# Kernel optimization log

Hardware: AMD Instinct MI355X
Metric: run time of the kernel (lower is better)

## Reference

```python
import jax, jax.numpy as jnp
import numpy as np

N_FILTERS = 1024
KH, KW = 5, 5
LOC = 3                      # locality (pad + maxpool kernel/stride)
B, H, W = 1024, 64, 64
WIN = KH + 2 * LOC           # 11: sliced window side after padding


def setup_inputs() -> dict:
    key = jax.random.key(0)
    k1, k2, k3, k4 = jax.random.split(key, 4)
    X = jax.random.normal(k1, (B, 1, H, W), dtype=jnp.float32)
    weight = jax.random.normal(k2, (N_FILTERS, 1, KH, KW), dtype=jnp.float32)
    bias = jax.random.normal(k3, (N_FILTERS,), dtype=jnp.float32)
    # top-left corner (i, j) of each filter's window in the padded image;
    # must satisfy i + KH + 2*LOC <= H + 2*LOC  =>  i in [0, H-KH]
    positions = jax.random.randint(k4, (N_FILTERS, 2), 0, H - KH + 1, dtype=jnp.int32)
    return {"X": X, "weight": weight, "bias": bias, "positions": positions}


def reference(X, weight, bias, positions):
    # ZeroPad2d(locality)
    Xp = jnp.pad(X, ((0, 0), (0, 0), (LOC, LOC), (LOC, LOC)))

    def slice_one(pos):
        return jax.lax.dynamic_slice(Xp, (0, 0, pos[0], pos[1]), (B, 1, WIN, WIN))

    windows = jax.vmap(slice_one)(positions)
    lhs = jnp.transpose(windows[:, :, 0], (1, 0, 2, 3))

    # All n_filters tiny single-channel convs as ONE grouped conv.
    conv = jax.lax.conv_general_dilated(
        lhs, weight, window_strides=(1, 1), padding='VALID',
        dimension_numbers=('NCHW', 'OIHW', 'NCHW'),
        feature_group_count=N_FILTERS)                # [B,F,2L+1,2L+1] = [B,F,7,7]
    conv = conv + bias[None, :, None, None]

    # MaxPool2d((LOC,LOC)) with default stride=LOC, floor mode -> 2x2.
    pooled = jax.lax.reduce_window(
        conv, -jnp.inf, jax.lax.max,
        window_dimensions=(1, 1, LOC, LOC),
        window_strides=(1, 1, LOC, LOC),
        padding='VALID')                              # [B,F,2,2]

    # torch.cat(dim=1) over per-filter [B,1,2,2] tensors + reshape(B,-1)
    return pooled.reshape(B, -1)                      # [B, F*4]
```

## Files before the change

kernel.cpp:

```cpp
#include <hip/hip_runtime.h>

#define N_FILTERS 1024
#define B_TOTAL   1024
#define IMG       64
#define PAD_DIM   70

typedef _Float16 half2_t __attribute__((ext_vector_type(2)));
typedef float    fvec2   __attribute__((ext_vector_type(2)));

__global__ __launch_bounds__(256) void prep_kernel(
    const float* __restrict__ X, _Float16* __restrict__ Xt)
{
    if (blockIdx.x < 512) {
        __shared__ float T[128 * 65];
        const int pt = blockIdx.x & 63;
        const int bt = blockIdx.x >> 6;
        const int tx = threadIdx.x & 63, ty = threadIdx.x >> 6;

        #pragma unroll
        for (int pass = 0; pass < 32; ++pass) {
            int bl = pass * 4 + ty;
            T[bl * 65 + tx] = X[(size_t)(bt * 128 + bl) * 4096 + pt * 64 + tx];
        }
        __syncthreads();
        #pragma unroll
        for (int pass = 0; pass < 16; ++pass) {
            int pl = pass * 4 + ty;
            int p  = pt * 64 + pl;
            int r  = p >> 6, c = p & 63;
            half2_t h;
            h.x = (_Float16)T[(2 * tx) * 65 + pl];
            h.y = (_Float16)T[(2 * tx + 1) * 65 + pl];
            *(half2_t*)&Xt[(size_t)((r + 3) * PAD_DIM + (c + 3)) * 1024 + bt * 128 + 2 * tx] = h;
        }
    } else {
        const int bp = blockIdx.x - 512;
        for (int pp = bp; pp < PAD_DIM * PAD_DIM; pp += 64) {
            int r = pp / PAD_DIM, c = pp - r * PAD_DIM;
            if (r >= 3 && r < 67 && c >= 3 && c < 67) continue;
            unsigned int* q = (unsigned int*)Xt + (size_t)pp * 512;
            q[threadIdx.x] = 0u;
            q[threadIdx.x + 256] = 0u;
        }
    }
}

__global__ __launch_bounds__(256, 2) void filters_main(
    const _Float16* __restrict__ Xt,
    const float*    __restrict__ W,
    const float*    __restrict__ bias,
    const int*      __restrict__ pos,
    float4*         __restrict__ out4)
{
    const int t    = threadIdx.x;
    const int lane = t & 63;
    const int w    = t >> 6;
    const int bg   = blockIdx.x & 3;
    const int fg   = blockIdx.x >> 2;

    const int f  = fg * 4 + w;
    const int sf = __builtin_amdgcn_readfirstlane(f);
    const int si = __builtin_amdgcn_readfirstlane(pos[2 * sf]);
    const int sj = __builtin_amdgcn_readfirstlane(pos[2 * sf + 1]);

    float wk[25];
    const float* wp = W + sf * 25;
    #pragma unroll
    for (int k = 0; k < 25; ++k) wk[k] = wp[k];

    const int laneByte = bg * 512 + lane * 8;

    fvec2 a0[36], a1[36];
    #pragma unroll
    for (int k = 0; k < 36; ++k) { a0[k] = (fvec2)0.0f; a1[k] = (fvec2)0.0f; }

    #pragma unroll
    for (int wr = 0; wr < 10; ++wr) {
        const char* rowp = (const char*)Xt
                         + (size_t)((si + wr) * PAD_DIM + sj) * 2048 + laneByte;
        fvec2 inA[10], inB[10];
        #pragma unroll
        for (int wc = 0; wc < 10; ++wc) {
            half2_t lo, hi;
            uint2 d = *(const uint2*)(rowp + (size_t)wc * 2048);
            lo = __builtin_bit_cast(half2_t, d.x);
            hi = __builtin_bit_cast(half2_t, d.y);
            inA[wc].x = (float)lo.x; inA[wc].y = (float)lo.y;
            inB[wc].x = (float)hi.x; inB[wc].y = (float)hi.y;
        }
        #pragma unroll
        for (int y = 0; y < 6; ++y) {
            if (y >= ((wr > 4) ? (wr - 4) : 0) && y <= ((wr < 5) ? wr : 5)) {
                const int r = wr - y;
                #pragma unroll
                for (int x = 0; x < 6; ++x) {
                    #pragma unroll
                    for (int c = 0; c < 5; ++c) {
                        a0[y * 6 + x] = wk[r * 5 + c] * inA[x + c] + a0[y * 6 + x];
                        a1[y * 6 + x] = wk[r * 5 + c] * inB[x + c] + a1[y * 6 + x];
                    }
                }
            }
        }
    }

    const float bv = bias[sf];
    float4 o0, o1;
    {
        fvec2 m0[4], m1[4];
        #pragma unroll
        for (int py = 0; py < 2; ++py) {
            #pragma unroll
            for (int px = 0; px < 2; ++px) {
                fvec2 u = a0[(3 * py) * 6 + 3 * px];
                fvec2 v = a1[(3 * py) * 6 + 3 * px];
                #pragma unroll
                for (int dy = 0; dy < 3; ++dy)
                    #pragma unroll
                    for (int dx = 0; dx < 3; ++dx) {
                        fvec2 e0 = a0[(3 * py + dy) * 6 + (3 * px + dx)];
                        fvec2 e1 = a1[(3 * py + dy) * 6 + (3 * px + dx)];
                        u.x = fmaxf(u.x, e0.x); u.y = fmaxf(u.y, e0.y);
                        v.x = fmaxf(v.x, e1.x); v.y = fmaxf(v.y, e1.y);
                    }
                m0[py * 2 + px].x = u.x + bv; m0[py * 2 + px].y = u.y + bv;
                m1[py * 2 + px].x = v.x + bv; m1[py * 2 + px].y = v.y + bv;
            }
        }
        const int b0 = bg * 256 + lane * 4;
        float4 o;
        o.x = m0[0].x; o.y = m0[1].x; o.z = m0[2].x; o.w = m0[3].x;
        out4[(size_t)b0 * 1024 + f] = o;
        o.x = m0[0].y; o.y = m0[1].y; o.z = m0[2].y; o.w = m0[3].y;
        out4[(size_t)(b0 + 1) * 1024 + f] = o;
        o.x = m1[0].x; o.y = m1[1].x; o.z = m1[2].x; o.w = m1[3].x;
        out4[(size_t)(b0 + 2) * 1024 + f] = o;
        o.x = m1[0].y; o.y = m1[1].y; o.z = m1[2].y; o.w = m1[3].y;
        out4[(size_t)(b0 + 3) * 1024 + f] = o;
        (void)o0; (void)o1;
    }
}

extern "C" void kernel_launch(void* const* d_in, const int* in_sizes, int n_in,
                              void* d_out, int out_size, void* d_ws, size_t ws_size,
                              hipStream_t stream) {
    const float* X    = (const float*)d_in[0];
    const float* W    = (const float*)d_in[1];
    const float* bias = (const float*)d_in[2];
    const int*   pos  = (const int*)d_in[3];
    float4* out4 = (float4*)d_out;
    _Float16* Xt = (_Float16*)d_ws;

    prep_kernel<<<576, 256, 0, stream>>>(X, Xt);
    filters_main<<<1024, 256, 0, stream>>>(Xt, W, bias, pos, out4);
}
```

Before: 104.1 us.

## Split pooled output rows across waves and halve batch per lane to cut registers

Each wave now computes a single pooled row (py) for one filter and 2 batch items per lane, where before it computed both pooled rows for 4 batch items. This cuts the accumulators from 72 float2 to 18 and allows 4 blocks per CU instead of 2, with the grid growing to 4096 blocks. The cost is redundant work: the convolution row ranges overlap (7 input rows per wave instead of 10 shared across both pooled rows), each batch-row load is smaller (4 bytes per lane), and the output stores become 8-byte writes.

```diff
diff --git a/kernel.cpp b/kernel.cpp
--- a/kernel.cpp
+++ b/kernel.cpp
@@ -45,100 +45,86 @@
     }
 }
 
-__global__ __launch_bounds__(256, 2) void filters_main(
+__global__ __launch_bounds__(256, 4) void filters_main(
     const _Float16* __restrict__ Xt,
     const float*    __restrict__ W,
     const float*    __restrict__ bias,
     const int*      __restrict__ pos,
-    float4*         __restrict__ out4)
+    float*          __restrict__ out)
 {
     const int t    = threadIdx.x;
     const int lane = t & 63;
-    const int w    = t >> 6;
-    const int bg   = blockIdx.x & 3;
-    const int fg   = blockIdx.x >> 2;
+    const int py   = (t >> 6) & 1;
+    const int fl   = t >> 7;
+    const int bg   = blockIdx.x & 7;
+    const int fg   = blockIdx.x >> 3;
 
-    const int f  = fg * 4 + w;
+    const int f  = fg * 2 + fl;
     const int sf = __builtin_amdgcn_readfirstlane(f);
     const int si = __builtin_amdgcn_readfirstlane(pos[2 * sf]);
     const int sj = __builtin_amdgcn_readfirstlane(pos[2 * sf + 1]);
+    const int r0 = si + 3 * py;
 
     float wk[25];
     const float* wp = W + sf * 25;
     #pragma unroll
     for (int k = 0; k < 25; ++k) wk[k] = wp[k];
 
-    const int laneByte = bg * 512 + lane * 8;
+    const int laneByte = bg * 256 + lane * 4;
 
-    fvec2 a0[36], a1[36];
+    fvec2 acc[18];
     #pragma unroll
-    for (int k = 0; k < 36; ++k) { a0[k] = (fvec2)0.0f; a1[k] = (fvec2)0.0f; }
+    for (int k = 0; k < 18; ++k) acc[k] = (fvec2)0.0f;
 
     #pragma unroll
-    for (int wr = 0; wr < 10; ++wr) {
+    for (int wrl = 0; wrl < 7; ++wrl) {
         const char* rowp = (const char*)Xt
-                         + (size_t)((si + wr) * PAD_DIM + sj) * 2048 + laneByte;
-        fvec2 inA[10], inB[10];
+                         + (size_t)((r0 + wrl) * PAD_DIM + sj) * 2048 + laneByte;
+        fvec2 in2[10];
         #pragma unroll
         for (int wc = 0; wc < 10; ++wc) {
-            half2_t lo, hi;
-            uint2 d = *(const uint2*)(rowp + (size_t)wc * 2048);
-            lo = __builtin_bit_cast(half2_t, d.x);
-            hi = __builtin_bit_cast(half2_t, d.y);
-            inA[wc].x = (float)lo.x; inA[wc].y = (float)lo.y;
-            inB[wc].x = (float)hi.x; inB[wc].y = (float)hi.y;
+            half2_t h = __builtin_bit_cast(half2_t,
+                          *(const unsigned int*)(rowp + (size_t)wc * 2048));
+            in2[wc].x = (float)h.x;
+            in2[wc].y = (float)h.y;
         }
         #pragma unroll
-        for (int y = 0; y < 6; ++y) {
-            if (y >= ((wr > 4) ? (wr - 4) : 0) && y <= ((wr < 5) ? wr : 5)) {
-                const int r = wr - y;
+        for (int y = 0; y < 3; ++y) {
+            if (y >= ((wrl > 4) ? (wrl - 4) : 0) && y <= ((wrl < 2) ? wrl : 2)) {
+                const int r = wrl - y;
                 #pragma unroll
                 for (int x = 0; x < 6; ++x) {
                     #pragma unroll
-                    for (int c = 0; c < 5; ++c) {
-                        a0[y * 6 + x] = wk[r * 5 + c] * inA[x + c] + a0[y * 6 + x];
-                        a1[y * 6 + x] = wk[r * 5 + c] * inB[x + c] + a1[y * 6 + x];
-                    }
+                    for (int c = 0; c < 5; ++c)
+                        acc[y * 6 + x] = wk[r * 5 + c] * in2[x + c] + acc[y * 6 + x];
                 }
             }
         }
     }
 
     const float bv = bias[sf];
-    float4 o0, o1;
-    {
-        fvec2 m0[4], m1[4];
+    fvec2 m[2];
+    #pragma unroll
+    for (int px = 0; px < 2; ++px) {
+        fvec2 u = acc[3 * px];
         #pragma unroll
-        for (int py = 0; py < 2; ++py) {
+        for (int y = 0; y < 3; ++y)
             #pragma unroll
-            for (int px = 0; px < 2; ++px) {
-                fvec2 u = a0[(3 * py) * 6 + 3 * px];
-                fvec2 v = a1[(3 * py) * 6 + 3 * px];
-                #pragma unroll
-                for (int dy = 0; dy < 3; ++dy)
-                    #pragma unroll
-                    for (int dx = 0; dx < 3; ++dx) {
-                        fvec2 e0 = a0[(3 * py + dy) * 6 + (3 * px + dx)];
-                        fvec2 e1 = a1[(3 * py + dy) * 6 + (3 * px + dx)];
-                        u.x = fmaxf(u.x, e0.x); u.y = fmaxf(u.y, e0.y);
-                        v.x = fmaxf(v.x, e1.x); v.y = fmaxf(v.y, e1.y);
-                    }
-                m0[py * 2 + px].x = u.x + bv; m0[py * 2 + px].y = u.y + bv;
-                m1[py * 2 + px].x = v.x + bv; m1[py * 2 + px].y = v.y + bv;
+            for (int dx = 0; dx < 3; ++dx) {
+                fvec2 e = acc[y * 6 + 3 * px + dx];
+                u.x = fmaxf(u.x, e.x);
+                u.y = fmaxf(u.y, e.y);
             }
-        }
-        const int b0 = bg * 256 + lane * 4;
-        float4 o;
-        o.x = m0[0].x; o.y = m0[1].x; o.z = m0[2].x; o.w = m0[3].x;
-        out4[(size_t)b0 * 1024 + f] = o;
-        o.x = m0[0].y; o.y = m0[1].y; o.z = m0[2].y; o.w = m0[3].y;
-        out4[(size_t)(b0 + 1) * 1024 + f] = o;
-        o.x = m1[0].x; o.y = m1[1].x; o.z = m1[2].x; o.w = m1[3].x;
-        out4[(size_t)(b0 + 2) * 1024 + f] = o;
-        o.x = m1[0].y; o.y = m1[1].y; o.z = m1[2].y; o.w = m1[3].y;
-        out4[(size_t)(b0 + 3) * 1024 + f] = o;
-        (void)o0; (void)o1;
+        m[px].x = u.x + bv;
+        m[px].y = u.y + bv;
     }
+
+    const int b0 = bg * 128 + lane * 2;
+    const size_t o0 = (size_t)b0 * 4096 + sf * 4 + py * 2;
+    fvec2 s0; s0.x = m[0].x; s0.y = m[1].x;
+    fvec2 s1; s1.x = m[0].y; s1.y = m[1].y;
+    *(fvec2*)&out[o0]        = s0;
+    *(fvec2*)&out[o0 + 4096] = s1;
 }
 
 extern "C" void kernel_launch(void* const* d_in, const int* in_sizes, int n_in,
@@ -148,9 +134,9 @@
     const float* W    = (const float*)d_in[1];
     const float* bias = (const float*)d_in[2];
     const int*   pos  = (const int*)d_in[3];
-    float4* out4 = (float4*)d_out;
+    float* out = (float*)d_out;
     _Float16* Xt = (_Float16*)d_ws;
 
     prep_kernel<<<576, 256, 0, stream>>>(X, Xt);
-    filters_main<<<1024, 256, 0, stream>>>(Xt, W, bias, pos, out4);
+    filters_main<<<4096, 256, 0, stream>>>(Xt, W, bias, pos, out);
 }
```

Result: no change. 104.5 us (+0.3%).
